# Performance work log

Hardware: AMD Instinct MI355X
Metric: run time of the kernel (lower is better)

The kernel has to match this reference:

```python
import jax, jax.numpy as jnp
import numpy as np
import math

B, T, C = 2, 1400, 256
H = 16
D = C // H            # 16
FF = 1024
VOCAB = 1400
SLOTS = 256
EPS = 1e-5


def _ln(x, g, b):
    m = jnp.mean(x, axis=-1, keepdims=True)
    v = jnp.mean(jnp.square(x - m), axis=-1, keepdims=True)
    return (x - m) * jax.lax.rsqrt(v + EPS) * g + b


def setup_inputs() -> dict:
    key = jax.random.key(0)
    ks = jax.random.split(key, 24)
    s = 0.02
    inp = {
        "x": jax.random.normal(ks[0], (B, T, C), dtype=jnp.float32),
        "disease_ids": jax.random.randint(ks[1], (B, T), 0, VOCAB),
        # nn.MultiheadAttention params (torch layout: [out,in])
        "in_proj_w": jax.random.normal(ks[2], (3 * C, C)) * s,
        "in_proj_b": jnp.zeros((3 * C,), jnp.float32),
        "out_proj_w": jax.random.normal(ks[3], (C, C)) * s,
        "out_proj_b": jnp.zeros((C,), jnp.float32),
        # LayerNorms
        "ln1_g": jnp.ones((C,), jnp.float32), "ln1_b": jnp.zeros((C,), jnp.float32),
        "ln2_g": jnp.ones((C,), jnp.float32), "ln2_b": jnp.zeros((C,), jnp.float32),
        "ln3_g": jnp.ones((C,), jnp.float32), "ln3_b": jnp.zeros((C,), jnp.float32),
        # DiseaseGraphAttention
        "gq_w": jax.random.normal(ks[4], (C, C)) * s, "gq_b": jnp.zeros((C,), jnp.float32),
        "gk_w": jax.random.normal(ks[5], (C, C)) * s, "gk_b": jnp.zeros((C,), jnp.float32),
        "gv_w": jax.random.normal(ks[6], (C, C)) * s, "gv_b": jnp.zeros((C,), jnp.float32),
        "go_w": jax.random.normal(ks[7], (C, C)) * s, "go_b": jnp.zeros((C,), jnp.float32),
        "affinity": jax.random.normal(ks[8], (VOCAB, VOCAB)) * 0.01,
        # LongTermMemoryBank (only the read path affects the returned output)
        "mem_bank": jax.random.normal(ks[9], (SLOTS, C)) * 0.1,
        "read_w": jax.random.normal(ks[10], (SLOTS, C)) * s,
        "read_b": jnp.zeros((SLOTS,), jnp.float32),
        # FFN
        "ffn_w1": jax.random.normal(ks[11], (FF, C)) * s, "ffn_b1": jnp.zeros((FF,), jnp.float32),
        "ffn_w2": jax.random.normal(ks[12], (C, FF)) * s, "ffn_b2": jnp.zeros((C,), jnp.float32),
    }
    return inp


def reference(x, disease_ids, in_proj_w, in_proj_b, out_proj_w, out_proj_b,
              ln1_g, ln1_b, ln2_g, ln2_b, ln3_g, ln3_b,
              gq_w, gq_b, gk_w, gk_b, gv_w, gv_b, go_w, go_b, affinity,
              mem_bank, read_w, read_b, ffn_w1, ffn_b1, ffn_w2, ffn_b2):
    scale = 1.0 / math.sqrt(D)

    # ---- standard MHA (pre-norm, residual), dropout in eval mode ----
    h = _ln(x, ln1_g, ln1_b)
    qkv = h @ in_proj_w.T + in_proj_b                      # [B,T,3C]
    q, k, v = jnp.split(qkv, 3, axis=-1)
    q = q.reshape(B, T, H, D); k = k.reshape(B, T, H, D); v = v.reshape(B, T, H, D)
    scores = jnp.einsum('bthd,bshd->bhts', q, k) * scale   # [B,H,T,T]
    attn = jax.nn.softmax(scores, axis=-1)
    o = jnp.einsum('bhts,bshd->bthd', attn, v).reshape(B, T, C)
    x = x + (o @ out_proj_w.T + out_proj_b)

    # ---- disease-graph attention with gathered affinity bias ----
    h = _ln(x, ln2_g, ln2_b)
    q = (h @ gq_w.T + gq_b).reshape(B, T, H, D)
    k = (h @ gk_w.T + gk_b).reshape(B, T, H, D)
    v = (h @ gv_w.T + gv_b).reshape(B, T, H, D)
    aff = affinity[disease_ids]                            # [B,T,VOCAB] (VOCAB == T)
    scores = jnp.einsum('bthd,bshd->bhts', q, k) * scale + aff[:, None, :, :] * 0.1
    attn = jax.nn.softmax(scores, axis=-1)
    o = jnp.einsum('bhts,bshd->bthd', attn, v).reshape(B, T, C)
    x = x + (o @ go_w.T + go_b)

    # ---- memory-bank read (write/erase only mutate params, not the output) ----
    read_weights = jax.nn.softmax(x @ read_w.T + read_b, axis=-1)   # [B,T,SLOTS]
    x = x + jnp.einsum('bts,sc->btc', read_weights, mem_bank)

    # ---- FFN ----
    h = _ln(x, ln3_g, ln3_b)
    ff = jax.nn.gelu(h @ ffn_w1.T + ffn_b1, approximate=False) @ ffn_w2.T + ffn_b2
    return x + ff
```

## Files before the change

### kernel.cpp

```cpp
#include <hip/hip_runtime.h>
#include <hip/hip_bf16.h>
#include <math.h>

namespace {

typedef __attribute__((ext_vector_type(4))) float f32x4;
typedef __attribute__((ext_vector_type(8))) short s16x8;
typedef __attribute__((ext_vector_type(4))) short s16x4;
typedef unsigned short ushort_t;

constexpr int kB = 2, kT = 1400, kC = 256, kH = 16, kFF = 1024;
constexpr int kBT = kB * kT;
constexpr float kEps = 1e-5f;
constexpr int kSP = 5;
constexpr int kSLen = 280;
constexpr int SBLK = 288;
constexpr int KPITCH = 24;
constexpr float kQScale   = 0.25f * 1.4426950408889634f;
constexpr float kAffScale = 0.1f * 1.4426950408889634f;

__device__ __forceinline__ ushort_t f2bf(float f) {
    unsigned u = __float_as_uint(f);
    u += 0x7fffu + ((u >> 16) & 1u);
    return (ushort_t)(u >> 16);
}
__device__ __forceinline__ float bf2f(ushort_t u) {
    return __uint_as_float(((unsigned)u) << 16);
}
__device__ __forceinline__ unsigned pk2bf(float a, float b) {
    __hip_bfloat162 t = __float22bfloat162_rn(make_float2(a, b));
    union { __hip_bfloat162 h; unsigned u; } cv; cv.h = t;
    return cv.u;
}
__device__ __forceinline__ float fast_exp2(float x) {
    float r;
    asm("v_exp_f32 %0, %1" : "=v"(r) : "v"(x));
    return r;
}

__global__ __launch_bounds__(256) void convert_kernel(
        const float* __restrict__ in_proj_w, const float* __restrict__ gq_w,
        const float* __restrict__ gk_w, const float* __restrict__ gv_w,
        const float* __restrict__ out_proj_w, const float* __restrict__ go_w,
        const float* __restrict__ ffn_w1, const float* __restrict__ ffn_w2,
        const float* __restrict__ read_w, const float* __restrict__ mem_bank,
        const float* __restrict__ gq_b, const float* __restrict__ gk_b,
        const float* __restrict__ gv_b,
        ushort_t* __restrict__ wdst, float* __restrict__ gqkvb) {
    const int bid = blockIdx.x, tid = threadIdx.x;
    if (bid == 608) {
        gqkvb[tid] = gq_b[tid];
        gqkvb[256 + tid] = gk_b[tid];
        gqkvb[512 + tid] = gv_b[tid];
        return;
    }
    const int u0 = (bid * 256 + tid) * 8;
    if (u0 >= 1114112) {
        #pragma unroll
        for (int j = 0; j < 8; j++) {
            const int d = u0 - 1114112 + j;
            wdst[1114112 + d] = f2bf(mem_bank[(d & 255) * 256 + (d >> 8)]);
        }
        return;
    }
    const float* src; int off;
    if      (u0 < 196608)  { src = in_proj_w;  off = u0; }
    else if (u0 < 262144)  { src = gq_w;       off = u0 - 196608; }
    else if (u0 < 327680)  { src = gk_w;       off = u0 - 262144; }
    else if (u0 < 393216)  { src = gv_w;       off = u0 - 327680; }
    else if (u0 < 458752)  { src = out_proj_w; off = u0 - 393216; }
    else if (u0 < 524288)  { src = go_w;       off = u0 - 458752; }
    else if (u0 < 786432)  { src = ffn_w1;     off = u0 - 524288; }
    else if (u0 < 1048576) { src = ffn_w2;     off = u0 - 786432; }
    else                   { src = read_w;     off = u0 - 1048576; }
    #pragma unroll
    for (int j = 0; j < 8; j++) wdst[u0 + j] = f2bf(src[off + j]);
}

__global__ __launch_bounds__(256) void ln_kernel(
        const float* __restrict__ x, const float* __restrict__ g,
        const float* __restrict__ b, ushort_t* __restrict__ out) {
    __shared__ float red[10];
    const int row = blockIdx.x, tid = threadIdx.x;
    const float v = x[row * kC + tid];
    float s1 = v, s2 = v * v;
    #pragma unroll
    for (int off = 32; off > 0; off >>= 1) {
        s1 += __shfl_down(s1, off);
        s2 += __shfl_down(s2, off);
    }
    if ((tid & 63) == 0) { red[tid >> 6] = s1; red[4 + (tid >> 6)] = s2; }
    __syncthreads();
    if (tid == 0) {
        red[8] = red[0] + red[1] + red[2] + red[3];
        red[9] = red[4] + red[5] + red[6] + red[7];
    }
    __syncthreads();
    const float mean = red[8] * (1.f / kC);
    const float var = red[9] * (1.f / kC) - mean * mean;
    out[row * kC + tid] = f2bf((v - mean) * rsqrtf(var + kEps) * g[tid] + b[tid]);
}

__global__ __launch_bounds__(256) void softmax256_kernel(
        const float* __restrict__ logits, ushort_t* __restrict__ probs) {
    __shared__ float red[5];
    const int row = blockIdx.x, tid = threadIdx.x;
    const float p = __expf(logits[row * 256 + tid]);
    float s = p;
    #pragma unroll
    for (int off = 32; off > 0; off >>= 1) s += __shfl_down(s, off);
    if ((tid & 63) == 0) red[tid >> 6] = s;
    __syncthreads();
    if (tid == 0) red[4] = red[0] + red[1] + red[2] + red[3];
    __syncthreads();
    probs[row * 256 + tid] = f2bf(p / red[4]);
}

__global__ __launch_bounds__(256) void gemm16_kernel(
        const ushort_t* __restrict__ A, const ushort_t* __restrict__ W,
        const float* __restrict__ bias, const float* __restrict__ res,
        float* __restrict__ outf, ushort_t* __restrict__ outb,
        ushort_t* __restrict__ outK, ushort_t* __restrict__ outV,
        int M, int N, int K, int ldo, int act, int mode) {
    __shared__ ushort_t dsA[64 * 64];
    __shared__ ushort_t dsW[64 * 64];
    const int tid = threadIdx.x;
    const int lane = tid & 63, wave = tid >> 6;
    const int qi = lane & 15, g = lane >> 4;
    const int wm = (wave >> 1) * 32, wn = (wave & 1) * 32;
    const int m0 = blockIdx.x * 64, n0 = blockIdx.y * 64;

    f32x4 acc[2][2] = {};
    for (int kt = 0; kt < K; kt += 64) {
        __syncthreads();
        #pragma unroll
        for (int j = 0; j < 2; ++j) {
            const int u = tid + j * 256;
            const int row = u >> 3, c = u & 7;
            const int cs = c ^ (row & 7);
            const int gmA = min(m0 + row, M - 1);
            *(s16x8*)&dsA[row * 64 + cs * 8] =
                *(const s16x8*)&A[(size_t)gmA * K + kt + c * 8];
            *(s16x8*)&dsW[row * 64 + cs * 8] =
                *(const s16x8*)&W[(size_t)(n0 + row) * K + kt + c * 8];
        }
        __syncthreads();
        #pragma unroll
        for (int kk = 0; kk < 2; ++kk) {
            s16x8 af[2], bf[2];
            #pragma unroll
            for (int f = 0; f < 2; ++f) {
                const int r = wm + f * 16 + qi;
                af[f] = *(const s16x8*)&dsA[r * 64 + (((kk * 4 + g) ^ (r & 7)) * 8)];
            }
            #pragma unroll
            for (int nn = 0; nn < 2; ++nn) {
                const int r = wn + nn * 16 + qi;
                bf[nn] = *(const s16x8*)&dsW[r * 64 + (((kk * 4 + g) ^ (r & 7)) * 8)];
            }
            #pragma unroll
            for (int f = 0; f < 2; ++f)
                #pragma unroll
                for (int nn = 0; nn < 2; ++nn)
                    acc[f][nn] = __builtin_amdgcn_mfma_f32_16x16x32_bf16(
                        af[f], bf[nn], acc[f][nn], 0, 0, 0);
        }
    }
    #pragma unroll
    for (int f = 0; f < 2; ++f) {
        #pragma unroll
        for (int r = 0; r < 4; ++r) {
            const int gm = m0 + wm + f * 16 + g * 4 + r;
            if (gm >= M) continue;
            #pragma unroll
            for (int nn = 0; nn < 2; ++nn) {
                const int gn = n0 + wn + nn * 16 + qi;
                float v = acc[f][nn][r];
                if (bias) v += bias[gn];
                if (act == 1) v = 0.5f * v * (1.f + erff(v * 0.70710678f));
                if (res) v += res[(size_t)gm * ldo + gn];
                if (mode == 1) {
                    const int bb = (gm >= kT) ? 1 : 0;
                    const int ss = gm - bb * kT;
                    const int hh = (gn & 255) >> 4, dd = gn & 15;
                    const size_t hoff = (((size_t)(bb * 16 + hh)) * kT + ss) * 16 + dd;
                    if (gn < 256)      outb[hoff] = f2bf(v * kQScale);
                    else if (gn < 512) outK[hoff] = f2bf(v);
                    else               outV[hoff] = f2bf(v);
                } else {
                    if (outf) outf[(size_t)gm * ldo + gn] = v;
                    if (outb) outb[(size_t)gm * ldo + gn] = f2bf(v);
                }
            }
        }
    }
}

template <bool kAff>
__global__ __launch_bounds__(512) void attn_mfma_kernel(
        const ushort_t* __restrict__ q, const ushort_t* __restrict__ kbuf,
        const ushort_t* __restrict__ vbuf, ushort_t* __restrict__ o_part,
        float* __restrict__ l_part,
        const float* __restrict__ affinity, const int* __restrict__ did) {
    __shared__ ushort_t ldsK[SBLK * KPITCH];
    __shared__ ushort_t ldsV[SBLK * 16];
    const int tid  = threadIdx.x;
    const int bid  = blockIdx.x;
    const int w    = (bid & 7) * 220 + (bid >> 3);
    const int slice = w / 11;
    const int ttile = w - slice * 11;
    const int h    = slice & 15;
    const int z    = slice >> 4;
    const int b    = (z >= 5) ? 1 : 0;
    const int sp   = z - b * 5;
    const int t0   = ttile * 128;
    const int s0   = sp * kSLen;
    const int lane = tid & 63;
    const int wave = tid >> 6;
    const int g    = lane >> 4;
    const int qi   = lane & 15;

    const int tq  = t0 + wave * 16 + qi;
    const int tqc = min(tq, kT - 1);
    const ushort_t* qhb = q + (size_t)(b * 16 + h) * kT * 16;
    s16x8 qb = {0, 0, 0, 0, 0, 0, 0, 0};
    if (g < 2) qb = *(const s16x8*)&qhb[(size_t)tqc * 16 + g * 8];
    const float* ar = nullptr;
    if (kAff) ar = affinity + (size_t)did[b * kT + tqc] * kT;

    const ushort_t* kb  = kbuf + (size_t)(b * 16 + h) * kT * 16;
    const ushort_t* vbp = vbuf + (size_t)(b * 16 + h) * kT * 16;
    for (int i = tid; i < SBLK * 2; i += 512) {
        const int sl = i >> 1, hf = i & 1;
        const int sg = min(s0 + sl, kT - 1);
        *(s16x8*)&ldsK[sl * KPITCH + hf * 8] =
            *(const s16x8*)&kb[(size_t)sg * 16 + hf * 8];
        *(s16x8*)&ldsV[sl * 16 + hf * 8] =
            *(const s16x8*)&vbp[(size_t)sg * 16 + hf * 8];
    }
    __syncthreads();

    f32x4 acc = {0.f, 0.f, 0.f, 0.f};
    float lrun = 0.f;
    const unsigned vaddr = (unsigned)(size_t)(&ldsV[0]) + lane * 8;
    s16x4 va0, va1;
    asm volatile("ds_read_b64_tr_b16 %0, %2\n\t"
                 "ds_read_b64_tr_b16 %1, %2 offset:512"
                 : "=&v"(va0), "=&v"(va1) : "v"(vaddr));

    #pragma unroll
    for (int c = 0; c < SBLK / 32; ++c) {
        const int sl0 = c * 32;
        const bool tail = (c == 8);
        const s16x8 ka0 = *(const s16x8*)&ldsK[(sl0 + qi) * KPITCH + (g & 1) * 8];
        const s16x8 ka1 = *(const s16x8*)&ldsK[(sl0 + 16 + qi) * KPITCH + (g & 1) * 8];
        const f32x4 z4 = {0.f, 0.f, 0.f, 0.f};
        f32x4 d0 = __builtin_amdgcn_mfma_f32_16x16x32_bf16(ka0, qb, z4, 0, 0, 0);
        f32x4 d1 = __builtin_amdgcn_mfma_f32_16x16x32_bf16(ka1, qb, z4, 0, 0, 0);
        float sv[8];
        #pragma unroll
        for (int r = 0; r < 4; r++) { sv[r] = d0[r]; sv[4 + r] = d1[r]; }
        if (kAff) {
            if (!tail) {
                const float4 a0 = *(const float4*)&ar[s0 + sl0 + 4 * g];
                const float4 a1 = *(const float4*)&ar[s0 + sl0 + 16 + 4 * g];
                sv[0] += kAffScale * a0.x; sv[1] += kAffScale * a0.y;
                sv[2] += kAffScale * a0.z; sv[3] += kAffScale * a0.w;
                sv[4] += kAffScale * a1.x; sv[5] += kAffScale * a1.y;
                sv[6] += kAffScale * a1.z; sv[7] += kAffScale * a1.w;
            } else {
                #pragma unroll
                for (int jj = 0; jj < 8; jj++) {
                    const int s_ = s0 + sl0 + 16 * (jj >> 2) + 4 * g + (jj & 3);
                    sv[jj] += kAffScale * ar[min(s_, kT - 1)];
                }
            }
        }
        float pv[8];
        #pragma unroll
        for (int jj = 0; jj < 8; jj++) pv[jj] = fast_exp2(sv[jj]);
        if (tail && g >= 2) { pv[4] = 0.f; pv[5] = 0.f; pv[6] = 0.f; pv[7] = 0.f; }
        lrun += ((pv[0] + pv[1]) + (pv[2] + pv[3])) + ((pv[4] + pv[5]) + (pv[6] + pv[7]));
        union { unsigned u[4]; s16x8 s; } pu;
        pu.u[0] = pk2bf(pv[0], pv[1]);
        pu.u[1] = pk2bf(pv[2], pv[3]);
        pu.u[2] = pk2bf(pv[4], pv[5]);
        pu.u[3] = pk2bf(pv[6], pv[7]);
        asm volatile("s_waitcnt lgkmcnt(0)" ::: "memory");
        __builtin_amdgcn_sched_barrier(0);
        s16x8 af;
        #pragma unroll
        for (int j = 0; j < 4; j++) { af[j] = va0[j]; af[4 + j] = va1[j]; }
        acc = __builtin_amdgcn_mfma_f32_16x16x32_bf16(af, pu.s, acc, 0, 0, 0);
        if (c < SBLK / 32 - 1) {
            asm volatile("ds_read_b64_tr_b16 %0, %2\n\t"
                         "ds_read_b64_tr_b16 %1, %2 offset:512"
                         : "=&v"(va0), "=&v"(va1) : "v"(vaddr + (sl0 + 32) * 32));
        }
    }
    lrun += __shfl_xor(lrun, 16);
    lrun += __shfl_xor(lrun, 32);
    const int slice_id = (b * kSP + sp) * 16 + h;
    if (lane < 16 && tq < kT)
        l_part[(size_t)slice_id * kT + tq] = lrun;
    ushort_t* ob = o_part + (size_t)slice_id * kT * 16;
    s16x4 ov;
    #pragma unroll
    for (int r = 0; r < 4; r++) ov[r] = (short)f2bf(acc[r]);
    if (tq < kT) *(s16x4*)&ob[(size_t)tq * 16 + 4 * g] = ov;
}

__global__ __launch_bounds__(256) void combine_kernel(
        const ushort_t* __restrict__ o_part, const float* __restrict__ l_part,
        ushort_t* __restrict__ o) {
    const int row = blockIdx.x, c = threadIdx.x;
    const int b = (row >= kT) ? 1 : 0, t = row - b * kT;
    const int h = c >> 4, d = c & 15;
    float l = 0.f, ov = 0.f;
    #pragma unroll
    for (int p = 0; p < kSP; ++p) {
        const int sl_ = (b * kSP + p) * 16 + h;
        l  += l_part[(size_t)sl_ * kT + t];
        ov += bf2f(o_part[((size_t)sl_ * kT + t) * 16 + d]);
    }
    o[(size_t)row * 256 + c] = f2bf(ov / l);
}

}

extern "C" void kernel_launch(void* const* d_in, const int* in_sizes, int n_in,
                              void* d_out, int out_size, void* d_ws, size_t ws_size,
                              hipStream_t stream) {
    const float* x          = (const float*)d_in[0];
    const int*   did        = (const int*)d_in[1];
    const float* in_proj_w  = (const float*)d_in[2];
    const float* in_proj_b  = (const float*)d_in[3];
    const float* out_proj_w = (const float*)d_in[4];
    const float* out_proj_b = (const float*)d_in[5];
    const float* ln1_g = (const float*)d_in[6];
    const float* ln1_b = (const float*)d_in[7];
    const float* ln2_g = (const float*)d_in[8];
    const float* ln2_b = (const float*)d_in[9];
    const float* ln3_g = (const float*)d_in[10];
    const float* ln3_b = (const float*)d_in[11];
    const float* gq_w = (const float*)d_in[12];
    const float* gq_b = (const float*)d_in[13];
    const float* gk_w = (const float*)d_in[14];
    const float* gk_b = (const float*)d_in[15];
    const float* gv_w = (const float*)d_in[16];
    const float* gv_b = (const float*)d_in[17];
    const float* go_w = (const float*)d_in[18];
    const float* go_b = (const float*)d_in[19];
    const float* affinity = (const float*)d_in[20];
    const float* mem_bank = (const float*)d_in[21];
    const float* read_w   = (const float*)d_in[22];
    const float* read_b   = (const float*)d_in[23];
    const float* ffn_w1 = (const float*)d_in[24];
    const float* ffn_b1 = (const float*)d_in[25];
    const float* ffn_w2 = (const float*)d_in[26];
    const float* ffn_b2 = (const float*)d_in[27];

    char* wsb = (char*)d_ws;
    ushort_t* o_part  = (ushort_t*)(wsb + 0);
    float*    l_part  = (float*)(wsb + 7168000);
    ushort_t* ff116   = (ushort_t*)(wsb + 8064000);
    float*    bufD    = (float*)(wsb + 13798400);
    ushort_t* bufA16  = (ushort_t*)(wsb + 16665600);
    float*    bufD2   = (float*)(wsb + 18099200);
    ushort_t* bufQ16  = (ushort_t*)(wsb + 20966400);
    ushort_t* bufK16  = (ushort_t*)(wsb + 22400000);
    ushort_t* bufV16  = (ushort_t*)(wsb + 23833600);
    ushort_t* o16     = (ushort_t*)(wsb + 25267200);
    ushort_t* wdst    = (ushort_t*)(wsb + 26700800);
    float*    gqkvb   = (float*)(wsb + 29191168);
    float*    logits  = (float*)(wsb + 20966400);
    ushort_t* probs16 = o16;
    ushort_t* bufD16  = bufA16;

    const ushort_t* wQKV1 = wdst;
    const ushort_t* wG    = wdst + 196608;
    const ushort_t* wO    = wdst + 393216;
    const ushort_t* wGO   = wdst + 458752;
    const ushort_t* wF1   = wdst + 524288;
    const ushort_t* wF2   = wdst + 786432;
    const ushort_t* wRead = wdst + 1048576;
    const ushort_t* wMemT = wdst + 1114112;

    const dim3 blk(256);
    const int MT = (kBT + 63) / 64;
    const dim3 g_qkv(MT, 12), g_c(MT, 4), g_ff(MT, 16);
    const dim3 g_at(11 * kH * kB * kSP);

    convert_kernel<<<609, blk, 0, stream>>>(in_proj_w, gq_w, gk_w, gv_w, out_proj_w,
                                            go_w, ffn_w1, ffn_w2, read_w, mem_bank,
                                            gq_b, gk_b, gv_b, wdst, gqkvb);
    ln_kernel<<<kBT, blk, 0, stream>>>(x, ln1_g, ln1_b, bufA16);
    gemm16_kernel<<<g_qkv, blk, 0, stream>>>(bufA16, wQKV1, in_proj_b, nullptr,
                                             nullptr, bufQ16, bufK16, bufV16,
                                             kBT, 768, kC, 768, 0, 1);
    attn_mfma_kernel<false><<<g_at, dim3(512), 0, stream>>>(bufQ16, bufK16, bufV16,
                                                            o_part, l_part,
                                                            nullptr, nullptr);
    combine_kernel<<<kBT, blk, 0, stream>>>(o_part, l_part, o16);
    gemm16_kernel<<<g_c, blk, 0, stream>>>(o16, wO, out_proj_b, x,
                                           bufD2, nullptr, nullptr, nullptr,
                                           kBT, kC, kC, kC, 0, 0);
    ln_kernel<<<kBT, blk, 0, stream>>>(bufD2, ln2_g, ln2_b, bufA16);
    gemm16_kernel<<<g_qkv, blk, 0, stream>>>(bufA16, wG, gqkvb, nullptr,
                                             nullptr, bufQ16, bufK16, bufV16,
                                             kBT, 768, kC, 768, 0, 1);
    attn_mfma_kernel<true><<<g_at, dim3(512), 0, stream>>>(bufQ16, bufK16, bufV16,
                                                           o_part, l_part,
                                                           affinity, did);
    combine_kernel<<<kBT, blk, 0, stream>>>(o_part, l_part, o16);
    gemm16_kernel<<<g_c, blk, 0, stream>>>(o16, wGO, go_b, bufD2,
                                           bufD, bufD16, nullptr, nullptr,
                                           kBT, kC, kC, kC, 0, 0);
    gemm16_kernel<<<g_c, blk, 0, stream>>>(bufD16, wRead, read_b, nullptr,
                                           logits, nullptr, nullptr, nullptr,
                                           kBT, kC, kC, kC, 0, 0);
    softmax256_kernel<<<kBT, blk, 0, stream>>>(logits, probs16);
    gemm16_kernel<<<g_c, blk, 0, stream>>>(probs16, wMemT, nullptr, bufD,
                                           bufD, nullptr, nullptr, nullptr,
                                           kBT, kC, kC, kC, 0, 0);
    ln_kernel<<<kBT, blk, 0, stream>>>(bufD, ln3_g, ln3_b, bufA16);
    gemm16_kernel<<<g_ff, blk, 0, stream>>>(bufA16, wF1, ffn_b1, nullptr,
                                            nullptr, ff116, nullptr, nullptr,
                                            kBT, kFF, kC, kFF, 1, 0);
    gemm16_kernel<<<g_c, blk, 0, stream>>>(ff116, wF2, ffn_b2, bufD,
                                           (float*)d_out, nullptr, nullptr, nullptr,
                                           kBT, kC, kFF, kC, 0, 0);
}
```

Before: 174.5 us.

## Fuse memory-bank read logits, softmax and readout GEMM into one kernel

Replaces the read-logits GEMM, the row softmax kernel and the memory-bank readout GEMM with a single kernel. Each block handles 16 rows: it converts x to bf16 in shared memory, computes logits with MFMA, exponentiates and sums them across waves, writes the unnormalised probabilities back to LDS, then multiplies by the transposed memory bank and applies the normalisation plus the residual in the epilogue. This removes two kernel launches and the global round-trips for the logits and probability buffers. In exchange the grid is only 175 blocks of 256 threads, which underfills the device, and weights are read straight from global memory without LDS staging.

```diff
diff --git a/kernel.cpp b/kernel.cpp
--- a/kernel.cpp
+++ b/kernel.cpp
@@ -99,21 +99,6 @@
     const float mean = red[8] * (1.f / kC);
     const float var = red[9] * (1.f / kC) - mean * mean;
     out[row * kC + tid] = f2bf((v - mean) * rsqrtf(var + kEps) * g[tid] + b[tid]);
-}
-
-__global__ __launch_bounds__(256) void softmax256_kernel(
-        const float* __restrict__ logits, ushort_t* __restrict__ probs) {
-    __shared__ float red[5];
-    const int row = blockIdx.x, tid = threadIdx.x;
-    const float p = __expf(logits[row * 256 + tid]);
-    float s = p;
-    #pragma unroll
-    for (int off = 32; off > 0; off >>= 1) s += __shfl_down(s, off);
-    if ((tid & 63) == 0) red[tid >> 6] = s;
-    __syncthreads();
-    if (tid == 0) red[4] = red[0] + red[1] + red[2] + red[3];
-    __syncthreads();
-    probs[row * 256 + tid] = f2bf(p / red[4]);
 }
 
 __global__ __launch_bounds__(256) void gemm16_kernel(
@@ -192,6 +177,105 @@
                     if (outb) outb[(size_t)gm * ldo + gn] = f2bf(v);
                 }
             }
+        }
+    }
+}
+
+__global__ __launch_bounds__(256) void memread_kernel(
+        const float* __restrict__ x2, const ushort_t* __restrict__ wRead,
+        const float* __restrict__ read_b, const ushort_t* __restrict__ wMemT,
+        float* __restrict__ xout) {
+    __shared__ ushort_t dsP[16 * 256];
+    __shared__ float lsum[4][16];
+    __shared__ float lt[16];
+    const int tid = threadIdx.x;
+    const int lane = tid & 63, wave = tid >> 6;
+    const int qi = lane & 15, g = lane >> 4;
+    const int wn = wave * 64;
+    const int m0 = blockIdx.x * 16;
+
+    {
+        const int r = tid >> 4, e = tid & 15;
+        const float* xr = x2 + (size_t)(m0 + r) * 256 + e * 16;
+        #pragma unroll
+        for (int i = 0; i < 2; i++) {
+            const float4 va = *(const float4*)&xr[i * 8];
+            const float4 vb = *(const float4*)&xr[i * 8 + 4];
+            union { unsigned u4[4]; s16x8 s; } pu;
+            pu.u4[0] = pk2bf(va.x, va.y);
+            pu.u4[1] = pk2bf(va.z, va.w);
+            pu.u4[2] = pk2bf(vb.x, vb.y);
+            pu.u4[3] = pk2bf(vb.z, vb.w);
+            const int cg = e * 2 + i;
+            *(s16x8*)&dsP[r * 256 + ((cg ^ (r & 7)) << 3)] = pu.s;
+        }
+    }
+    __syncthreads();
+    f32x4 acc[4] = {};
+    for (int kt = 0; kt < 8; ++kt) {
+        const int cg = kt * 4 + g;
+        const s16x8 af = *(const s16x8*)&dsP[qi * 256 + ((cg ^ (qi & 7)) << 3)];
+        #pragma unroll
+        for (int nn = 0; nn < 4; ++nn) {
+            const int wr = wn + nn * 16 + qi;
+            const s16x8 bf = *(const s16x8*)&wRead[(size_t)wr * 256 + kt * 32 + g * 8];
+            acc[nn] = __builtin_amdgcn_mfma_f32_16x16x32_bf16(af, bf, acc[nn], 0, 0, 0);
+        }
+    }
+    float p[4][4];
+    float rs[4] = {0.f, 0.f, 0.f, 0.f};
+    #pragma unroll
+    for (int nn = 0; nn < 4; ++nn) {
+        const float bb = read_b[wn + nn * 16 + qi];
+        #pragma unroll
+        for (int r = 0; r < 4; ++r) {
+            p[nn][r] = __expf(acc[nn][r] + bb);
+            rs[r] += p[nn][r];
+        }
+    }
+    #pragma unroll
+    for (int r = 0; r < 4; ++r) {
+        rs[r] += __shfl_xor(rs[r], 1);
+        rs[r] += __shfl_xor(rs[r], 2);
+        rs[r] += __shfl_xor(rs[r], 4);
+        rs[r] += __shfl_xor(rs[r], 8);
+    }
+    __syncthreads();
+    if (qi == 0) {
+        #pragma unroll
+        for (int r = 0; r < 4; ++r) lsum[wave][4 * g + r] = rs[r];
+    }
+    #pragma unroll
+    for (int nn = 0; nn < 4; ++nn) {
+        #pragma unroll
+        for (int r = 0; r < 4; ++r) {
+            const int row = 4 * g + r, col = wn + nn * 16 + qi;
+            const int cg = col >> 3, e = col & 7;
+            dsP[row * 256 + ((cg ^ (row & 7)) << 3) + e] = f2bf(p[nn][r]);
+        }
+    }
+    __syncthreads();
+    if (tid < 16)
+        lt[tid] = 1.f / (lsum[0][tid] + lsum[1][tid] + lsum[2][tid] + lsum[3][tid]);
+    __syncthreads();
+    f32x4 acc2[4] = {};
+    for (int kt = 0; kt < 8; ++kt) {
+        const int cg = kt * 4 + g;
+        const s16x8 af = *(const s16x8*)&dsP[qi * 256 + ((cg ^ (qi & 7)) << 3)];
+        #pragma unroll
+        for (int nn = 0; nn < 4; ++nn) {
+            const int wr = wn + nn * 16 + qi;
+            const s16x8 bf = *(const s16x8*)&wMemT[(size_t)wr * 256 + kt * 32 + g * 8];
+            acc2[nn] = __builtin_amdgcn_mfma_f32_16x16x32_bf16(af, bf, acc2[nn], 0, 0, 0);
+        }
+    }
+    #pragma unroll
+    for (int nn = 0; nn < 4; ++nn) {
+        #pragma unroll
+        for (int r = 0; r < 4; ++r) {
+            const int row = 4 * g + r;
+            const size_t idx = (size_t)(m0 + row) * 256 + wn + nn * 16 + qi;
+            xout[idx] = acc2[nn][r] * lt[row] + x2[idx];
         }
     }
 }
@@ -373,9 +457,6 @@
     ushort_t* o16     = (ushort_t*)(wsb + 25267200);
     ushort_t* wdst    = (ushort_t*)(wsb + 26700800);
     float*    gqkvb   = (float*)(wsb + 29191168);
-    float*    logits  = (float*)(wsb + 20966400);
-    ushort_t* probs16 = o16;
-    ushort_t* bufD16  = bufA16;
 
     const ushort_t* wQKV1 = wdst;
     const ushort_t* wG    = wdst + 196608;
@@ -414,15 +495,9 @@
                                                            affinity, did);
     combine_kernel<<<kBT, blk, 0, stream>>>(o_part, l_part, o16);
     gemm16_kernel<<<g_c, blk, 0, stream>>>(o16, wGO, go_b, bufD2,
-                                           bufD, bufD16, nullptr, nullptr,
-                                           kBT, kC, kC, kC, 0, 0);
-    gemm16_kernel<<<g_c, blk, 0, stream>>>(bufD16, wRead, read_b, nullptr,
-                                           logits, nullptr, nullptr, nullptr,
-                                           kBT, kC, kC, kC, 0, 0);
-    softmax256_kernel<<<kBT, blk, 0, stream>>>(logits, probs16);
-    gemm16_kernel<<<g_c, blk, 0, stream>>>(probs16, wMemT, nullptr, bufD,
                                            bufD, nullptr, nullptr, nullptr,
                                            kBT, kC, kC, kC, 0, 0);
+    memread_kernel<<<kBT / 16, blk, 0, stream>>>(bufD, wRead, read_b, wMemT, bufD);
     ln_kernel<<<kBT, blk, 0, stream>>>(bufD, ln3_g, ln3_b, bufA16);
     gemm16_kernel<<<g_ff, blk, 0, stream>>>(bufA16, wF1, ffn_b1, nullptr,
                                             nullptr, ff116, nullptr, nullptr,
```

Result: faster. 162.5 us (-6.9%).
